# Kernel tuning notes

Measured on AMD Instinct MI355X. Metric: run time of the kernel, lower is better.

Reference implementation:

```python
import jax, jax.numpy as jnp
import numpy as np

D_MODEL, N_HEAD, D_HEAD = 192, 12, 16
S, B, RLEN = 1024, 4, 2048
LN_EPS = 1e-12


def _xavier(key, shape):
    fan_in, fan_out = shape[0], int(np.prod(shape[1:]))
    limit = float(np.sqrt(6.0 / (fan_in + fan_out)))
    return jax.random.uniform(key, shape, jnp.float32, -limit, limit)


def setup_inputs() -> dict:
    key = jax.random.key(0)
    ks = jax.random.split(key, 12)
    inp = {
        "x": jax.random.normal(ks[0], (S, B, D_MODEL), jnp.float32),
        "r": jax.random.normal(ks[1], (RLEN, B, D_MODEL), jnp.float32),
        "mask0": jnp.zeros((S, S, B, 1), jnp.float32),
        "Wq": _xavier(ks[2], (D_MODEL, N_HEAD, D_HEAD)),
        "Wk": _xavier(ks[3], (D_MODEL, N_HEAD, D_HEAD)),
        "Wv": _xavier(ks[4], (D_MODEL, N_HEAD, D_HEAD)),
        "Wo": _xavier(ks[5], (D_MODEL, N_HEAD, D_HEAD)),
        "Wr": _xavier(ks[6], (D_MODEL, N_HEAD, D_HEAD)),
        "r_w_bias": _xavier(ks[7], (N_HEAD, D_HEAD)),
        "r_r_bias": _xavier(ks[8], (N_HEAD, D_HEAD)),
        "ln_w": jnp.ones((D_MODEL,), jnp.float32),
        "ln_b": jnp.zeros((D_MODEL,), jnp.float32),
    }
    return inp


def _rel_shift_bnij(x, klen):
    # x: [b, n, i, j] with j = rlen; XLNet relative shift, keep first klen cols
    b, n, i, j = x.shape
    x = x.reshape(b, n, j, i)[:, :, 1:, :].reshape(b, n, i, j - 1)
    return x[:, :, :, :klen]


def reference(x, r, mask0, Wq, Wk, Wv, Wo, Wr, r_w_bias, r_r_bias, ln_w, ln_b):
    mask0 = jnp.zeros_like(mask0)  # Model.forward zeroes the mask
    q_head = jnp.einsum("ibh,hnd->ibnd", x, Wq)
    k_head = jnp.einsum("ibh,hnd->ibnd", x, Wk)
    v_head = jnp.einsum("ibh,hnd->ibnd", x, Wv)
    k_head_r = jnp.einsum("ibh,hnd->ibnd", r, Wr)

    # content-based score
    ac = jnp.einsum("ibnd,jbnd->bnij", q_head + r_w_bias, k_head)
    # position-based score with relative shift
    bd = jnp.einsum("ibnd,jbnd->bnij", q_head + r_r_bias, k_head_r)
    bd = _rel_shift_bnij(bd, ac.shape[3])
    # seg_mat is None -> segment term ef = 0

    scale = 1.0 / np.sqrt(D_HEAD)
    attn_score = (ac + bd) * scale
    attn_score = attn_score - 1e30 * jnp.einsum("ijbn->bnij", mask0)
    attn_prob = jax.nn.softmax(attn_score, axis=3)

    attn_vec = jnp.einsum("bnij,jbnd->ibnd", attn_prob, v_head)
    attn_out = jnp.einsum("ibnd,hnd->ibh", attn_vec, Wo)

    out = attn_out + x  # residual
    mean = jnp.mean(out, axis=-1, keepdims=True)
    var = jnp.mean(jnp.square(out - mean), axis=-1, keepdims=True)
    out = (out - mean) * jax.lax.rsqrt(var + LN_EPS) * ln_w + ln_b
    return out
```

## Files before the change

### kernel.cpp

```cpp
#include <hip/hip_runtime.h>
#include <hip/hip_bf16.h>

#define SQ   1024
#define BB   4
#define DM   192
#define NH   12
#define DH   16
#define RL   2048
#define BN   (BB*NH)

typedef __attribute__((ext_vector_type(8))) short  short8;
typedef __attribute__((ext_vector_type(4))) float  f32x4;
typedef __attribute__((ext_vector_type(2))) unsigned u32x2;
typedef __attribute__((ext_vector_type(4))) unsigned u32x4;

__device__ __forceinline__ short f2bf(float f) {
    unsigned u = __float_as_uint(f);
    u += 0x7fff + ((u >> 16) & 1);
    return (short)(u >> 16);
}
__device__ __forceinline__ unsigned pkbf(float lo, float hi) {
    union { __hip_bfloat162 h; unsigned u; } cv;
    cv.h = __float22bfloat162_rn(make_float2(lo, hi));
    return cv.u;
}
__device__ __forceinline__ short8 as_s8(u32x4 v) {
    union { u32x4 u; short8 s; } c; c.u = v; return c.s;
}
#define P32SWAP(a, b) asm volatile("v_permlane32_swap_b32 %0, %1" : "+v"(a), "+v"(b))
#define P16SWAP(a, b) asm volatile("v_permlane16_swap_b32 %0, %1" : "+v"(a), "+v"(b))

__global__ __launch_bounds__(256) void k_prep(
    const float* __restrict__ x, const float* __restrict__ r,
    const float* __restrict__ Wq, const float* __restrict__ Wk,
    const float* __restrict__ Wv, const float* __restrict__ Wr,
    const float* __restrict__ Wo,
    unsigned short* __restrict__ xb, unsigned short* __restrict__ rb,
    unsigned short* __restrict__ WTq, unsigned short* __restrict__ WTk,
    unsigned short* __restrict__ WTv, unsigned short* __restrict__ WTr,
    unsigned short* __restrict__ Wob)
{
    int idx = blockIdx.x * 256 + threadIdx.x;
    if (idx < 786432) { xb[idx] = (unsigned short)f2bf(x[idx]); return; }
    idx -= 786432;
    if (idx < 1572864) { rb[idx] = (unsigned short)f2bf(r[idx]); return; }
    idx -= 1572864;
    if (idx < 36864) { int nd = idx / 192, h = idx % 192;
                       WTq[idx] = (unsigned short)f2bf(Wq[h*192 + nd]); return; }
    idx -= 36864;
    if (idx < 36864) { int nd = idx / 192, h = idx % 192;
                       WTk[idx] = (unsigned short)f2bf(Wk[h*192 + nd]); return; }
    idx -= 36864;
    if (idx < 36864) { int nd = idx / 192, h = idx % 192;
                       WTv[idx] = (unsigned short)f2bf(Wv[h*192 + nd]); return; }
    idx -= 36864;
    if (idx < 36864) { int nd = idx / 192, h = idx % 192;
                       WTr[idx] = (unsigned short)f2bf(Wr[h*192 + nd]); return; }
    idx -= 36864;
    if (idx < 36864) { Wob[idx] = (unsigned short)f2bf(Wo[idx]); return; }
}

__global__ __launch_bounds__(256) void k_gemm_xr(
    const unsigned short* __restrict__ xb, const unsigned short* __restrict__ rbm,
    const unsigned short* __restrict__ WTq, const unsigned short* __restrict__ WTk,
    const unsigned short* __restrict__ WTv, const unsigned short* __restrict__ WTr,
    const float* __restrict__ rwb, const float* __restrict__ rrb,
    unsigned short* __restrict__ qwb, unsigned short* __restrict__ qrb,
    unsigned short* __restrict__ kh, unsigned short* __restrict__ vh,
    unsigned short* __restrict__ kr)
{
    int bid = blockIdx.x;
    int tid = threadIdx.x, w = tid >> 6, lane = tid & 63, g = lane >> 4, mm = lane & 15;
    if (bid < 1152) {
        int rt2 = bid / 9, ch = bid % 9;
        int wsel = ch / 3, sub = ch % 3;
        int c0 = sub * 64 + w * 16;
        const unsigned short* WT = (wsel == 0) ? WTq : ((wsel == 1) ? WTk : WTv);
        const unsigned short* arow0 = xb + (size_t)(rt2*32 + mm) * 192 + 8*g;
        const unsigned short* arow1 = arow0 + 16*192;
        const unsigned short* brow = WT + (size_t)(c0 + mm) * 192 + 8*g;
        f32x4 acc0 = {0.f,0.f,0.f,0.f}, acc1 = {0.f,0.f,0.f,0.f};
        #pragma unroll
        for (int kk = 0; kk < 6; ++kk) {
            short8 b  = *(const short8*)(brow  + kk*32);
            short8 a0 = *(const short8*)(arow0 + kk*32);
            short8 a1 = *(const short8*)(arow1 + kk*32);
            acc0 = __builtin_amdgcn_mfma_f32_16x16x32_bf16(a0, b, acc0, 0, 0, 0);
            acc1 = __builtin_amdgcn_mfma_f32_16x16x32_bf16(a1, b, acc1, 0, 0, 0);
        }
        int col = c0 + mm, n = col >> 4, d = col & 15;
        if (wsel == 0) {
            const float SCL = 0.3606737602222409f;
            float bw = rwb[col], br = rrb[col];
            #pragma unroll
            for (int r = 0; r < 4; ++r) {
                int row = rt2*32 + 4*g + r;
                int i = row >> 2, b2 = row & 3;
                size_t o = ((size_t)(b2*NH + n) * SQ + i) * DH + d;
                qwb[o] = (unsigned short)f2bf((acc0[r] + bw) * SCL);
                qrb[o] = (unsigned short)f2bf((acc0[r] + br) * SCL);
                int row1 = row + 16;
                int i1 = row1 >> 2, b21 = row1 & 3;
                size_t o1 = ((size_t)(b21*NH + n) * SQ + i1) * DH + d;
                qwb[o1] = (unsigned short)f2bf((acc1[r] + bw) * SCL);
                qrb[o1] = (unsigned short)f2bf((acc1[r] + br) * SCL);
            }
        } else {
            unsigned short* dst = (wsel == 1) ? kh : vh;
            #pragma unroll
            for (int r = 0; r < 4; ++r) {
                int row = rt2*32 + 4*g + r;
                int i = row >> 2, b2 = row & 3;
                dst[((size_t)(b2*NH + n) * SQ + i) * DH + d] = (unsigned short)f2bf(acc0[r]);
                int row1 = row + 16;
                int i1 = row1 >> 2, b21 = row1 & 3;
                dst[((size_t)(b21*NH + n) * SQ + i1) * DH + d] = (unsigned short)f2bf(acc1[r]);
            }
        }
    } else {
        int bb = bid - 1152;
        int rt2 = bb / 3, sub = bb % 3;
        int c0 = sub * 64 + w * 16;
        const unsigned short* arow0 = rbm + (size_t)(rt2*32 + mm) * 192 + 8*g;
        const unsigned short* arow1 = arow0 + 16*192;
        const unsigned short* brow = WTr + (size_t)(c0 + mm) * 192 + 8*g;
        f32x4 acc0 = {0.f,0.f,0.f,0.f}, acc1 = {0.f,0.f,0.f,0.f};
        #pragma unroll
        for (int kk = 0; kk < 6; ++kk) {
            short8 b  = *(const short8*)(brow  + kk*32);
            short8 a0 = *(const short8*)(arow0 + kk*32);
            short8 a1 = *(const short8*)(arow1 + kk*32);
            acc0 = __builtin_amdgcn_mfma_f32_16x16x32_bf16(a0, b, acc0, 0, 0, 0);
            acc1 = __builtin_amdgcn_mfma_f32_16x16x32_bf16(a1, b, acc1, 0, 0, 0);
        }
        int col = c0 + mm, n = col >> 4, d = col & 15;
        #pragma unroll
        for (int r = 0; r < 4; ++r) {
            int row = rt2*32 + 4*g + r;
            int j = row >> 2, b2 = row & 3;
            kr[((size_t)(b2*NH + n) * RL + j) * DH + d] = (unsigned short)f2bf(acc0[r]);
            int row1 = row + 16;
            int j1 = row1 >> 2, b21 = row1 & 3;
            kr[((size_t)(b21*NH + n) * RL + j1) * DH + d] = (unsigned short)f2bf(acc1[r]);
        }
    }
}

__global__ __launch_bounds__(256, 3) void k_attn_mfma(
    const unsigned short* __restrict__ qwb, const unsigned short* __restrict__ qrb,
    const unsigned short* __restrict__ kh, const unsigned short* __restrict__ vh,
    const unsigned short* __restrict__ kr, unsigned short* __restrict__ av_b)
{
    __shared__ __align__(16) short vbuf[2][64*16];
    __shared__ __align__(16) float bdls[4][16*84];

    int bid = blockIdx.x;
    int logical = (bid & 7) * 96 + (bid >> 3);
    int bn = logical >> 4;
    int i0b = (logical & 15) * 64;
    int tid = threadIdx.x, w = tid >> 6, lane = tid & 63;
    int g = lane >> 4, mm = lane & 15;
    size_t headK = (size_t)bn * SQ * DH;
    size_t headR = (size_t)bn * RL * DH;
    int koff = 8 * (g & 1);

    short8 qwf = {0,0,0,0,0,0,0,0}, qrf = {0,0,0,0,0,0,0,0};
    if (g < 2) {
        int qrow = i0b + 16*w + mm;
        qwf = *(const short8*)((const short*)qwb + headK + (size_t)qrow*DH + 8*g);
        qrf = *(const short8*)((const short*)qrb + headK + (size_t)qrow*DH + 8*g);
    }

    if (tid < 128) {
        int rr2 = tid >> 1, hh = tid & 1;
        *(u32x4*)(&vbuf[0][rr2*16 + hh*8]) =
            *(const u32x4*)(vh + headK + (size_t)rr2*16 + hh*8);
    }
    const int basew0 = 1008 - i0b - 16*w;
    u32x4 ka[4], krg[5], kan[4], krn[5];
    #pragma unroll
    for (int tp = 0; tp < 4; ++tp)
        ka[tp] = *(const u32x4*)(kh + headK + (size_t)(16*tp + mm)*16 + koff);
    #pragma unroll
    for (int tau = 0; tau < 5; ++tau)
        krg[tau] = *(const u32x4*)(kr + headR + (size_t)(basew0 + 16*tau + mm)*16 + koff);
    __syncthreads();

    float Lacc = 0.f;
    f32x4 opv = {0.f,0.f,0.f,0.f};
    float* bw_ = &bdls[w][0];
    const f32x4 z = {0.f,0.f,0.f,0.f};

    for (int t = 0; t < 16; ++t) {
        int cur = t & 1;
        u32x4 sva = {0,0,0,0}, svb = {0,0,0,0};
        bool ds = (t < 15);
        if (ds) {
            #pragma unroll
            for (int tp = 0; tp < 4; ++tp)
                kan[tp] = *(const u32x4*)(kh + headK + (size_t)(64*(t+1) + 16*tp + mm)*16 + koff);
            #pragma unroll
            for (int tau = 0; tau < 5; ++tau)
                krn[tau] = *(const u32x4*)(kr + headR + (size_t)(basew0 + 64*(t+1) + 16*tau + mm)*16 + koff);
            if (w == 1) {
                const unsigned short* p = vh + headK + (size_t)(64*(t+1) + lane)*16;
                sva = *(const u32x4*)p; svb = *(const u32x4*)(p + 8);
            }
        }

        #pragma unroll
        for (int tau = 0; tau < 5; ++tau) {
            f32x4 bd = __builtin_amdgcn_mfma_f32_16x16x32_bf16(as_s8(krg[tau]), qrf, z, 0, 0, 0);
            *(f32x4*)(bw_ + mm*84 + 16*tau + 4*g) = bd;
        }

        unsigned pk[8]; float Lc = 0.f;
        #pragma unroll
        for (int tp = 0; tp < 4; ++tp) {
            f32x4 ac = __builtin_amdgcn_mfma_f32_16x16x32_bf16(as_s8(ka[tp]), qwf, z, 0, 0, 0);
            int cb = mm*84 + 16*tp + 4*g + 16 - mm;
            float p0 = __builtin_amdgcn_exp2f(ac[0] + bw_[cb + 0]);
            float p1 = __builtin_amdgcn_exp2f(ac[1] + bw_[cb + 1]);
            float p2 = __builtin_amdgcn_exp2f(ac[2] + bw_[cb + 2]);
            float p3 = __builtin_amdgcn_exp2f(ac[3] + bw_[cb + 3]);
            Lc += (p0 + p1) + (p2 + p3);
            pk[2*tp]     = pkbf(p0, p1);
            pk[2*tp + 1] = pkbf(p2, p3);
        }
        Lacc += Lc;

        P32SWAP(pk[0], pk[2]); P16SWAP(pk[0], pk[2]);
        P32SWAP(pk[1], pk[3]); P16SWAP(pk[1], pk[3]);
        P32SWAP(pk[4], pk[6]); P16SWAP(pk[4], pk[6]);
        P32SWAP(pk[5], pk[7]); P16SWAP(pk[5], pk[7]);

        unsigned vb0 = (unsigned)(size_t)(&vbuf[cur][0])
                     + ((unsigned)mm << 3) + ((unsigned)g << 8);
        {
            u32x2 t0, t1;
            asm volatile("ds_read_b64_tr_b16 %0, %2 offset:0\n\t"
                         "ds_read_b64_tr_b16 %1, %2 offset:128\n\t"
                         "s_waitcnt lgkmcnt(0)"
                         : "=&v"(t0), "=&v"(t1) : "v"(vb0));
            __builtin_amdgcn_sched_barrier(0);
            union { unsigned u[4]; short8 s; } va, pb;
            va.u[0]=t0[0]; va.u[1]=t0[1]; va.u[2]=t1[0]; va.u[3]=t1[1];
            pb.u[0]=pk[0]; pb.u[1]=pk[1]; pb.u[2]=pk[2]; pb.u[3]=pk[3];
            opv = __builtin_amdgcn_mfma_f32_16x16x32_bf16(va.s, pb.s, opv, 0, 0, 0);
        }
        {
            u32x2 t0, t1;
            asm volatile("ds_read_b64_tr_b16 %0, %2 offset:0\n\t"
                         "ds_read_b64_tr_b16 %1, %2 offset:128\n\t"
                         "s_waitcnt lgkmcnt(0)"
                         : "=&v"(t0), "=&v"(t1) : "v"(vb0 + 1024));
            __builtin_amdgcn_sched_barrier(0);
            union { unsigned u[4]; short8 s; } va, pb;
            va.u[0]=t0[0]; va.u[1]=t0[1]; va.u[2]=t1[0]; va.u[3]=t1[1];
            pb.u[0]=pk[4]; pb.u[1]=pk[5]; pb.u[2]=pk[6]; pb.u[3]=pk[7];
            opv = __builtin_amdgcn_mfma_f32_16x16x32_bf16(va.s, pb.s, opv, 0, 0, 0);
        }

        if (ds) {
            if (w == 1) {
                *(u32x4*)(&vbuf[cur^1][lane*16])     = sva;
                *(u32x4*)(&vbuf[cur^1][lane*16 + 8]) = svb;
            }
        }
        __syncthreads();
        if (ds) {
            #pragma unroll
            for (int tp = 0; tp < 4; ++tp) ka[tp] = kan[tp];
            #pragma unroll
            for (int tau = 0; tau < 5; ++tau) krg[tau] = krn[tau];
        }
    }

    Lacc += __shfl_xor(Lacc, 16);
    Lacc += __shfl_xor(Lacc, 32);
    float inv = 1.0f / Lacc;
    int b2 = bn / NH, nn = bn % NH;
    int i = i0b + 16*w + mm;
    unsigned o0 = pkbf(opv[0]*inv, opv[1]*inv);
    unsigned o1 = pkbf(opv[2]*inv, opv[3]*inv);
    u32x2 ov = {o0, o1};
    *(u32x2*)(av_b + ((size_t)i*4 + b2)*192 + nn*16 + 4*g) = ov;
}

__global__ __launch_bounds__(256) void k_out_ln(
    const unsigned short* __restrict__ avb, const unsigned short* __restrict__ Wob,
    const float* __restrict__ x,
    const float* __restrict__ lnw, const float* __restrict__ lnb,
    float* __restrict__ out)
{
    __shared__ __align__(16) float os[16][196];
    int tid = threadIdx.x, w = tid >> 6, lane = tid & 63, g = lane >> 4, mm = lane & 15;
    int rt = blockIdx.x;
    const unsigned short* arow = avb + (size_t)(rt*16 + mm)*192 + 8*g;
    short8 a[6];
    #pragma unroll
    for (int kk = 0; kk < 6; ++kk) a[kk] = *(const short8*)(arow + kk*32);
    #pragma unroll
    for (int s = 0; s < 3; ++s) {
        int c0 = w*48 + s*16;
        const unsigned short* brow = Wob + (size_t)(c0 + mm)*192 + 8*g;
        f32x4 acc = {0.f,0.f,0.f,0.f};
        #pragma unroll
        for (int kk = 0; kk < 6; ++kk) {
            short8 b = *(const short8*)(brow + kk*32);
            acc = __builtin_amdgcn_mfma_f32_16x16x32_bf16(a[kk], b, acc, 0, 0, 0);
        }
        int col = c0 + mm;
        #pragma unroll
        for (int r = 0; r < 4; ++r) {
            int rl = 4*g + r;
            os[rl][col] = acc[r] + x[(size_t)(rt*16 + rl)*192 + col];
        }
    }
    __syncthreads();
    int row = tid >> 4, seg = tid & 15;
    const float* ors = &os[row][0] + seg*12;
    f32x4 v0 = *(const f32x4*)(ors);
    f32x4 v1 = *(const f32x4*)(ors + 4);
    f32x4 v2 = *(const f32x4*)(ors + 8);
    float s1 = ((v0[0]+v0[1])+(v0[2]+v0[3])) + ((v1[0]+v1[1])+(v1[2]+v1[3]))
             + ((v2[0]+v2[1])+(v2[2]+v2[3]));
    float q1 = ((v0[0]*v0[0]+v0[1]*v0[1])+(v0[2]*v0[2]+v0[3]*v0[3]))
             + ((v1[0]*v1[0]+v1[1]*v1[1])+(v1[2]*v1[2]+v1[3]*v1[3]))
             + ((v2[0]*v2[0]+v2[1]*v2[1])+(v2[2]*v2[2]+v2[3]*v2[3]));
    #pragma unroll
    for (int off = 1; off < 16; off <<= 1) {
        s1 += __shfl_xor(s1, off);
        q1 += __shfl_xor(q1, off);
    }
    float mean = s1 * (1.0f / 192.0f);
    float var  = q1 * (1.0f / 192.0f) - mean * mean;
    float rstd = rsqrtf(var + 1e-12f);
    int c0 = seg * 12;
    size_t ro = (size_t)(rt*16 + row) * 192;
    #pragma unroll
    for (int c = 0; c < 12; ++c) {
        float v = (c < 4) ? v0[c] : ((c < 8) ? v1[c-4] : v2[c-8]);
        out[ro + c0 + c] = (v - mean) * rstd * lnw[c0 + c] + lnb[c0 + c];
    }
}

extern "C" void kernel_launch(void* const* d_in, const int* in_sizes, int n_in,
                              void* d_out, int out_size, void* d_ws, size_t ws_size,
                              hipStream_t stream) {
    const float* x   = (const float*)d_in[0];
    const float* r   = (const float*)d_in[1];
    const float* Wq  = (const float*)d_in[3];
    const float* Wk  = (const float*)d_in[4];
    const float* Wv  = (const float*)d_in[5];
    const float* Wo  = (const float*)d_in[6];
    const float* Wr  = (const float*)d_in[7];
    const float* rwb = (const float*)d_in[8];
    const float* rrb = (const float*)d_in[9];
    const float* lnw = (const float*)d_in[10];
    const float* lnb = (const float*)d_in[11];
    float* out = (float*)d_out;

    char* ws = (char*)d_ws;
    unsigned short* qwb = (unsigned short*)(ws + 0);
    unsigned short* qrb = (unsigned short*)(ws + 1572864);
    unsigned short* kh  = (unsigned short*)(ws + 3145728);
    unsigned short* vh  = (unsigned short*)(ws + 4718592);
    unsigned short* kr  = (unsigned short*)(ws + 6291456);
    unsigned short* avb = (unsigned short*)(ws + 9437184);
    unsigned short* xb  = (unsigned short*)(ws + 11010048);
    unsigned short* rb  = (unsigned short*)(ws + 12582912);
    unsigned short* WTq = (unsigned short*)(ws + 15728640);
    unsigned short* WTk = (unsigned short*)(ws + 15802368);
    unsigned short* WTv = (unsigned short*)(ws + 15876096);
    unsigned short* WTr = (unsigned short*)(ws + 15949824);
    unsigned short* Wob = (unsigned short*)(ws + 16023552);

    k_prep<<<dim3(9936), dim3(256), 0, stream>>>(x, r, Wq, Wk, Wv, Wr, Wo,
                                                 xb, rb, WTq, WTk, WTv, WTr, Wob);
    k_gemm_xr<<<dim3(1920), dim3(256), 0, stream>>>(xb, rb, WTq, WTk, WTv, WTr,
                                                    rwb, rrb, qwb, qrb, kh, vh, kr);
    k_attn_mfma<<<dim3(768), dim3(256), 0, stream>>>(qwb, qrb, kh, vh, kr, avb);
    k_out_ln<<<dim3(256), dim3(256), 0, stream>>>(avb, Wob, x, lnw, lnb, out);
}
```

Baseline: 64.85 us.

## Fuse x/r bf16 conversion into projection GEMM and drop attention block barriers

The projection GEMM now reads fp32 x and r directly and converts them to bf16 in registers, so the prep kernel only transposes and converts the weights. This removes a large elementwise pass and its round trip of intermediate bf16 copies through memory. In the attention kernel, each wave now keeps its own double-buffered V tile in shared memory and loads it itself. That removes both __syncthreads calls, at the cost of four times more V loads and LDS use per block, which could lower occupancy. The GEMM also reads twice the A-operand bytes, and each x/r tile is converted again by every block that uses it.

```diff
diff --git a/kernel.cpp b/kernel.cpp
--- a/kernel.cpp
+++ b/kernel.cpp
@@ -27,24 +27,25 @@
 __device__ __forceinline__ short8 as_s8(u32x4 v) {
     union { u32x4 u; short8 s; } c; c.u = v; return c.s;
 }
+__device__ __forceinline__ short8 ldcvt(const float* p) {
+    f32x4 lo = *(const f32x4*)p, hi = *(const f32x4*)(p + 4);
+    union { unsigned u[4]; short8 s; } c;
+    c.u[0] = pkbf(lo[0], lo[1]); c.u[1] = pkbf(lo[2], lo[3]);
+    c.u[2] = pkbf(hi[0], hi[1]); c.u[3] = pkbf(hi[2], hi[3]);
+    return c.s;
+}
 #define P32SWAP(a, b) asm volatile("v_permlane32_swap_b32 %0, %1" : "+v"(a), "+v"(b))
 #define P16SWAP(a, b) asm volatile("v_permlane16_swap_b32 %0, %1" : "+v"(a), "+v"(b))
 
 __global__ __launch_bounds__(256) void k_prep(
-    const float* __restrict__ x, const float* __restrict__ r,
     const float* __restrict__ Wq, const float* __restrict__ Wk,
     const float* __restrict__ Wv, const float* __restrict__ Wr,
     const float* __restrict__ Wo,
-    unsigned short* __restrict__ xb, unsigned short* __restrict__ rb,
     unsigned short* __restrict__ WTq, unsigned short* __restrict__ WTk,
     unsigned short* __restrict__ WTv, unsigned short* __restrict__ WTr,
     unsigned short* __restrict__ Wob)
 {
     int idx = blockIdx.x * 256 + threadIdx.x;
-    if (idx < 786432) { xb[idx] = (unsigned short)f2bf(x[idx]); return; }
-    idx -= 786432;
-    if (idx < 1572864) { rb[idx] = (unsigned short)f2bf(r[idx]); return; }
-    idx -= 1572864;
     if (idx < 36864) { int nd = idx / 192, h = idx % 192;
                        WTq[idx] = (unsigned short)f2bf(Wq[h*192 + nd]); return; }
     idx -= 36864;
@@ -61,7 +62,7 @@
 }
 
 __global__ __launch_bounds__(256) void k_gemm_xr(
-    const unsigned short* __restrict__ xb, const unsigned short* __restrict__ rbm,
+    const float* __restrict__ x, const float* __restrict__ rm,
     const unsigned short* __restrict__ WTq, const unsigned short* __restrict__ WTk,
     const unsigned short* __restrict__ WTv, const unsigned short* __restrict__ WTr,
     const float* __restrict__ rwb, const float* __restrict__ rrb,
@@ -76,15 +77,15 @@
         int wsel = ch / 3, sub = ch % 3;
         int c0 = sub * 64 + w * 16;
         const unsigned short* WT = (wsel == 0) ? WTq : ((wsel == 1) ? WTk : WTv);
-        const unsigned short* arow0 = xb + (size_t)(rt2*32 + mm) * 192 + 8*g;
-        const unsigned short* arow1 = arow0 + 16*192;
+        const float* arow0 = x + (size_t)(rt2*32 + mm) * 192 + 8*g;
+        const float* arow1 = arow0 + 16*192;
         const unsigned short* brow = WT + (size_t)(c0 + mm) * 192 + 8*g;
         f32x4 acc0 = {0.f,0.f,0.f,0.f}, acc1 = {0.f,0.f,0.f,0.f};
         #pragma unroll
         for (int kk = 0; kk < 6; ++kk) {
-            short8 b  = *(const short8*)(brow  + kk*32);
-            short8 a0 = *(const short8*)(arow0 + kk*32);
-            short8 a1 = *(const short8*)(arow1 + kk*32);
+            short8 b  = *(const short8*)(brow + kk*32);
+            short8 a0 = ldcvt(arow0 + kk*32);
+            short8 a1 = ldcvt(arow1 + kk*32);
             acc0 = __builtin_amdgcn_mfma_f32_16x16x32_bf16(a0, b, acc0, 0, 0, 0);
             acc1 = __builtin_amdgcn_mfma_f32_16x16x32_bf16(a1, b, acc1, 0, 0, 0);
         }
@@ -121,15 +122,15 @@
         int bb = bid - 1152;
         int rt2 = bb / 3, sub = bb % 3;
         int c0 = sub * 64 + w * 16;
-        const unsigned short* arow0 = rbm + (size_t)(rt2*32 + mm) * 192 + 8*g;
-        const unsigned short* arow1 = arow0 + 16*192;
+        const float* arow0 = rm + (size_t)(rt2*32 + mm) * 192 + 8*g;
+        const float* arow1 = arow0 + 16*192;
         const unsigned short* brow = WTr + (size_t)(c0 + mm) * 192 + 8*g;
         f32x4 acc0 = {0.f,0.f,0.f,0.f}, acc1 = {0.f,0.f,0.f,0.f};
         #pragma unroll
         for (int kk = 0; kk < 6; ++kk) {
-            short8 b  = *(const short8*)(brow  + kk*32);
-            short8 a0 = *(const short8*)(arow0 + kk*32);
-            short8 a1 = *(const short8*)(arow1 + kk*32);
+            short8 b  = *(const short8*)(brow + kk*32);
+            short8 a0 = ldcvt(arow0 + kk*32);
+            short8 a1 = ldcvt(arow1 + kk*32);
             acc0 = __builtin_amdgcn_mfma_f32_16x16x32_bf16(a0, b, acc0, 0, 0, 0);
             acc1 = __builtin_amdgcn_mfma_f32_16x16x32_bf16(a1, b, acc1, 0, 0, 0);
         }
@@ -151,7 +152,7 @@
     const unsigned short* __restrict__ kh, const unsigned short* __restrict__ vh,
     const unsigned short* __restrict__ kr, unsigned short* __restrict__ av_b)
 {
-    __shared__ __align__(16) short vbuf[2][64*16];
+    __shared__ __align__(16) short vbuf[4][2][64*16];
     __shared__ __align__(16) float bdls[4][16*84];
 
     int bid = blockIdx.x;
@@ -171,10 +172,11 @@
         qrf = *(const short8*)((const short*)qrb + headK + (size_t)qrow*DH + 8*g);
     }
 
-    if (tid < 128) {
-        int rr2 = tid >> 1, hh = tid & 1;
-        *(u32x4*)(&vbuf[0][rr2*16 + hh*8]) =
-            *(const u32x4*)(vh + headK + (size_t)rr2*16 + hh*8);
+    {
+        const unsigned short* p = vh + headK + (size_t)lane*16;
+        u32x4 a0 = *(const u32x4*)p, a1 = *(const u32x4*)(p + 8);
+        *(u32x4*)(&vbuf[w][0][lane*16])     = a0;
+        *(u32x4*)(&vbuf[w][0][lane*16 + 8]) = a1;
     }
     const int basew0 = 1008 - i0b - 16*w;
     u32x4 ka[4], krg[5], kan[4], krn[5];
@@ -184,7 +186,6 @@
     #pragma unroll
     for (int tau = 0; tau < 5; ++tau)
         krg[tau] = *(const u32x4*)(kr + headR + (size_t)(basew0 + 16*tau + mm)*16 + koff);
-    __syncthreads();
 
     float Lacc = 0.f;
     f32x4 opv = {0.f,0.f,0.f,0.f};
@@ -202,10 +203,8 @@
             #pragma unroll
             for (int tau = 0; tau < 5; ++tau)
                 krn[tau] = *(const u32x4*)(kr + headR + (size_t)(basew0 + 64*(t+1) + 16*tau + mm)*16 + koff);
-            if (w == 1) {
-                const unsigned short* p = vh + headK + (size_t)(64*(t+1) + lane)*16;
-                sva = *(const u32x4*)p; svb = *(const u32x4*)(p + 8);
-            }
+            const unsigned short* p = vh + headK + (size_t)(64*(t+1) + lane)*16;
+            sva = *(const u32x4*)p; svb = *(const u32x4*)(p + 8);
         }
 
         #pragma unroll
@@ -234,7 +233,7 @@
         P32SWAP(pk[4], pk[6]); P16SWAP(pk[4], pk[6]);
         P32SWAP(pk[5], pk[7]); P16SWAP(pk[5], pk[7]);
 
-        unsigned vb0 = (unsigned)(size_t)(&vbuf[cur][0])
+        unsigned vb0 = (unsigned)(size_t)(&vbuf[w][cur][0])
                      + ((unsigned)mm << 3) + ((unsigned)g << 8);
         {
             u32x2 t0, t1;
@@ -262,13 +261,8 @@
         }
 
         if (ds) {
-            if (w == 1) {
-                *(u32x4*)(&vbuf[cur^1][lane*16])     = sva;
-                *(u32x4*)(&vbuf[cur^1][lane*16 + 8]) = svb;
-            }
-        }
-        __syncthreads();
-        if (ds) {
+            *(u32x4*)(&vbuf[w][cur^1][lane*16])     = sva;
+            *(u32x4*)(&vbuf[w][cur^1][lane*16 + 8]) = svb;
             #pragma unroll
             for (int tp = 0; tp < 4; ++tp) ka[tp] = kan[tp];
             #pragma unroll
@@ -368,17 +362,15 @@
     unsigned short* vh  = (unsigned short*)(ws + 4718592);
     unsigned short* kr  = (unsigned short*)(ws + 6291456);
     unsigned short* avb = (unsigned short*)(ws + 9437184);
-    unsigned short* xb  = (unsigned short*)(ws + 11010048);
-    unsigned short* rb  = (unsigned short*)(ws + 12582912);
-    unsigned short* WTq = (unsigned short*)(ws + 15728640);
-    unsigned short* WTk = (unsigned short*)(ws + 15802368);
-    unsigned short* WTv = (unsigned short*)(ws + 15876096);
-    unsigned short* WTr = (unsigned short*)(ws + 15949824);
-    unsigned short* Wob = (unsigned short*)(ws + 16023552);
-
-    k_prep<<<dim3(9936), dim3(256), 0, stream>>>(x, r, Wq, Wk, Wv, Wr, Wo,
-                                                 xb, rb, WTq, WTk, WTv, WTr, Wob);
-    k_gemm_xr<<<dim3(1920), dim3(256), 0, stream>>>(xb, rb, WTq, WTk, WTv, WTr,
+    unsigned short* WTq = (unsigned short*)(ws + 11010048);
+    unsigned short* WTk = (unsigned short*)(ws + 11083776);
+    unsigned short* WTv = (unsigned short*)(ws + 11157504);
+    unsigned short* WTr = (unsigned short*)(ws + 11231232);
+    unsigned short* Wob = (unsigned short*)(ws + 11304960);
+
+    k_prep<<<dim3(720), dim3(256), 0, stream>>>(Wq, Wk, Wv, Wr, Wo,
+                                                WTq, WTk, WTv, WTr, Wob);
+    k_gemm_xr<<<dim3(1920), dim3(256), 0, stream>>>(x, r, WTq, WTk, WTv, WTr,
                                                     rwb, rrb, qwb, qrb, kh, vh, kr);
     k_attn_mfma<<<dim3(768), dim3(256), 0, stream>>>(qwb, qrb, kh, vh, kr, avb);
     k_out_ln<<<dim3(256), dim3(256), 0, stream>>>(avb, Wob, x, lnw, lnb, out);
```

Measured after the change: 70.22 us. 1.08x slower.
